# Optimization experiments

Measured on AMD Instinct MI355X. Metric: run time of the kernel, lower is better.

The kernel has to match this reference:

```python
import jax, jax.numpy as jnp
import numpy as np

N = 100000      # nodes
E = 800000      # edges (avg degree 8)
D_IN = 256      # input feature dim
D_H = 256       # hidden dim (hard-coded in module)
D_OUT = 128     # h_feats


def setup_inputs() -> dict:
    key = jax.random.key(0)
    ks = jax.random.split(key, 8)
    feat = jax.random.normal(ks[0], (N, D_IN), jnp.float32)
    src = jax.random.randint(ks[1], (E,), 0, N, dtype=jnp.int32)
    dst = jax.random.randint(ks[2], (E,), 0, N, dtype=jnp.int32)
    def lin(k, din, dout):
        return jax.random.normal(k, (din, dout), jnp.float32) / np.float32(np.sqrt(din))
    return {
        'feat': feat, 'src': src, 'dst': dst,
        'w_self1': lin(ks[3], D_IN, D_H), 'w_neigh1': lin(ks[4], D_IN, D_H),
        'b1': jnp.zeros((D_H,), jnp.float32),
        'w_self2': lin(ks[5], D_H, D_OUT), 'w_neigh2': lin(ks[6], D_H, D_OUT),
        'b2': jnp.zeros((D_OUT,), jnp.float32),
    }


def _sage_mean(h, src, dst, w_self, w_neigh, b):
    # DGL SAGEConv 'mean': rst = h @ W_self + mean_{in-neighbors}(h) @ W_neigh + b
    ones = jnp.ones((src.shape[0],), h.dtype)
    deg = jax.ops.segment_sum(ones, dst, num_segments=N)          # in-degree per node
    msum = jax.ops.segment_sum(h[src], dst, num_segments=N)      # [N, d] gather-scatter
    mean = msum / jnp.maximum(deg, 1.0)[:, None]                  # zero-degree -> 0
    return h @ w_self + mean @ w_neigh + b


def reference(feat, src, dst, w_self1, w_neigh1, b1, w_self2, w_neigh2, b2):
    h = jax.nn.relu(_sage_mean(feat, src, dst, w_self1, w_neigh1, b1))
    h = jax.nn.relu(_sage_mean(h, src, dst, w_self2, w_neigh2, b2))
    # F.normalize(h, dim=1): x / max(||x||_2, eps)
    norm = jnp.linalg.norm(h, axis=1, keepdims=True)
    return h / jnp.maximum(norm, 1e-12)
```

## Files before the change

### kernel.cpp

```cpp
#include <hip/hip_runtime.h>

#define DIN 256
#define DH  256
#define DOUT 128

typedef __attribute__((ext_vector_type(8))) short bf16x8;
typedef __attribute__((ext_vector_type(4))) float f32x4;
typedef __attribute__((ext_vector_type(2))) float f32x2;
typedef __attribute__((ext_vector_type(4))) unsigned short ushort4v;
typedef __attribute__((ext_vector_type(8))) unsigned short ushort8v;
typedef __attribute__((ext_vector_type(4))) unsigned int uint4v;

static __device__ __forceinline__ unsigned short f2bf(float x) {
    unsigned u = __float_as_uint(x);
    u += 0x7fffu + ((u >> 16) & 1u);
    return (unsigned short)(u >> 16);
}
static __device__ __forceinline__ float bf2f(unsigned short h) {
    return __uint_as_float(((unsigned)h) << 16);
}

static __device__ __forceinline__ void gload16(const unsigned short* g, void* l) {
    __builtin_amdgcn_global_load_lds(
        (const __attribute__((address_space(1))) unsigned int*)g,
        (__attribute__((address_space(3))) unsigned int*)l,
        16, 0, 0);
}

__global__ void prep_kernel(const float* __restrict__ feat, unsigned short* __restrict__ featb,
                            unsigned int* __restrict__ feat8, long long nc4,
                            const float* __restrict__ w_self1, const float* __restrict__ w_neigh1,
                            const float* __restrict__ w_self2, const float* __restrict__ w_neigh2,
                            unsigned short* __restrict__ ws1t, unsigned short* __restrict__ wn1t,
                            unsigned short* __restrict__ wcat,
                            const int* __restrict__ dst, int* __restrict__ cnt, int E,
                            int bCvt, int bWt) {
    int b = blockIdx.x;
    if (b < bCvt) {
        long long i = b * 256LL + threadIdx.x;
        if (i >= nc4) return;
        f32x4 v = __builtin_nontemporal_load((const f32x4*)feat + i);
        ushort4v o;
        o[0] = f2bf(v[0]); o[1] = f2bf(v[1]); o[2] = f2bf(v[2]); o[3] = f2bf(v[3]);
        *((ushort4v*)featb + i) = o;
        int u = __builtin_amdgcn_cvt_pk_fp8_f32(v[0], v[1], 0, 0);
        u     = __builtin_amdgcn_cvt_pk_fp8_f32(v[2], v[3], u, 1);
        feat8[i] = (unsigned)u;
    } else if (b < bCvt + bWt) {
        int idx = (b - bCvt) * 256 + threadIdx.x;
        if (idx < 65536) {
            int nn = idx >> 8, k = idx & 255;
            ws1t[idx] = f2bf(w_self1[k * 256 + nn]);
        } else if (idx < 131072) {
            int j = idx - 65536; int nn = j >> 8, k = j & 255;
            wn1t[j] = f2bf(w_neigh1[k * 256 + nn]);
        } else if (idx < 163840) {
            int j = idx - 131072; int nn = j >> 8, k = j & 255;
            wcat[j] = f2bf(w_neigh2[k * 128 + nn]);
        } else if (idx < 196608) {
            int j = idx - 163840; int nn = j >> 8, k = j & 255;
            wcat[32768 + j] = f2bf(w_self2[k * 128 + nn]);
        }
    } else {
        int e = (b - bCvt - bWt) * 256 + threadIdx.x;
        if (e < E) atomicAdd(&cnt[dst[e]], 1);
    }
}

__global__ void block_sums_kernel(const int* __restrict__ cnt, int* __restrict__ partial, int N) {
    __shared__ int sdata[256];
    int t = threadIdx.x;
    int base = blockIdx.x * 1024;
    int s = 0;
#pragma unroll
    for (int j = 0; j < 4; ++j) {
        int i = base + t * 4 + j;
        if (i < N) s += cnt[i];
    }
    sdata[t] = s; __syncthreads();
    for (int o = 128; o; o >>= 1) {
        if (t < o) sdata[t] += sdata[t + o];
        __syncthreads();
    }
    if (t == 0) partial[blockIdx.x] = sdata[0];
}

__global__ void scan_partials_kernel(int* __restrict__ partial, int nb) {
    __shared__ int sdata[256];
    int t = threadIdx.x;
    int v = (t < nb) ? partial[t] : 0;
    sdata[t] = v; __syncthreads();
    for (int o = 1; o < 256; o <<= 1) {
        int y = (t >= o) ? sdata[t - o] : 0;
        __syncthreads();
        sdata[t] += y;
        __syncthreads();
    }
    if (t < nb) partial[t] = sdata[t] - v;
}

__global__ void scan_block_kernel(int* __restrict__ cnt, const int* __restrict__ partial,
                                  int* __restrict__ off, int N, int E) {
    __shared__ int sdata[256];
    int b = blockIdx.x, t = threadIdx.x;
    int base = b * 1024;
    int vals[4]; int local = 0;
#pragma unroll
    for (int j = 0; j < 4; ++j) {
        int i = base + t * 4 + j;
        vals[j] = (i < N) ? cnt[i] : 0;
        local += vals[j];
    }
    sdata[t] = local; __syncthreads();
    for (int o = 1; o < 256; o <<= 1) {
        int y = (t >= o) ? sdata[t - o] : 0;
        __syncthreads();
        sdata[t] += y;
        __syncthreads();
    }
    int run = sdata[t] - local + partial[b];
#pragma unroll
    for (int j = 0; j < 4; ++j) {
        int i = base + t * 4 + j;
        if (i < N) { off[i] = run; cnt[i] = run; }
        run += vals[j];
    }
    if (b == 0 && t == 0) off[N] = E;
}

__global__ void fill_csr_kernel(const int* __restrict__ src, const int* __restrict__ dst,
                                int* __restrict__ cursor, int* __restrict__ csr, int E) {
    int e = blockIdx.x * blockDim.x + threadIdx.x;
    if (e < E) {
        int d = dst[e];
        int p = atomicAdd(&cursor[d], 1);
        csr[p] = src[e];
    }
}

__global__ void gather_mean256_kernel(const unsigned int* __restrict__ feat8, const int* __restrict__ off,
                                      const int* __restrict__ csr, unsigned short* __restrict__ agg, int N) {
    int wid  = (int)((blockIdx.x * (long long)blockDim.x + threadIdx.x) >> 6);
    int lane = threadIdx.x & 63;
    if (wid >= N) return;
    int start = off[wid], end = off[wid + 1];
    const int g   = lane >> 4;
    const int cl  = lane & 15;
    float a[16] = {};
    int e = start;
    for (; e + 7 < end; e += 8) {
        int s0 = csr[e + g], s1 = csr[e + 4 + g];
        uint4v v0 = *(const uint4v*)(feat8 + (long long)s0 * 64 + cl * 4);
        uint4v v1 = *(const uint4v*)(feat8 + (long long)s1 * 64 + cl * 4);
#pragma unroll
        for (int d = 0; d < 4; ++d) {
            f32x2 p0 = __builtin_amdgcn_cvt_pk_f32_fp8((int)v0[d], false);
            f32x2 p1 = __builtin_amdgcn_cvt_pk_f32_fp8((int)v0[d], true);
            f32x2 q0 = __builtin_amdgcn_cvt_pk_f32_fp8((int)v1[d], false);
            f32x2 q1 = __builtin_amdgcn_cvt_pk_f32_fp8((int)v1[d], true);
            a[d * 4 + 0] += p0[0] + q0[0];
            a[d * 4 + 1] += p0[1] + q0[1];
            a[d * 4 + 2] += p1[0] + q1[0];
            a[d * 4 + 3] += p1[1] + q1[1];
        }
    }
    for (; e < end; e += 4) {
        int idx = e + g;
        if (idx < end) {
            int s = csr[idx];
            uint4v v = *(const uint4v*)(feat8 + (long long)s * 64 + cl * 4);
#pragma unroll
            for (int d = 0; d < 4; ++d) {
                f32x2 p0 = __builtin_amdgcn_cvt_pk_f32_fp8((int)v[d], false);
                f32x2 p1 = __builtin_amdgcn_cvt_pk_f32_fp8((int)v[d], true);
                a[d * 4 + 0] += p0[0];
                a[d * 4 + 1] += p0[1];
                a[d * 4 + 2] += p1[0];
                a[d * 4 + 3] += p1[1];
            }
        }
    }
#pragma unroll
    for (int j = 0; j < 16; ++j) {
        a[j] += __shfl_xor(a[j], 16);
        a[j] += __shfl_xor(a[j], 32);
    }
    if (g == 0) {
        float inv = 1.0f / (float)max(end - start, 1);
        ushort8v o0, o1;
#pragma unroll
        for (int j = 0; j < 8; ++j) { o0[j] = f2bf(a[j] * inv); o1[j] = f2bf(a[8 + j] * inv); }
        unsigned short* dstp = agg + (long long)wid * 256 + cl * 16;
        *(ushort8v*)dstp       = o0;
        *(ushort8v*)(dstp + 8) = o1;
    }
}

__global__ __launch_bounds__(512)
void gemm1_kernel(const unsigned short* __restrict__ A,  const unsigned short* __restrict__ WT,
                  const unsigned short* __restrict__ A2, const unsigned short* __restrict__ WT2,
                  const float* __restrict__ bias, unsigned short* __restrict__ C, int M)
{
    const int K = 256;
    __shared__ __align__(16) char lds[2][24576];

    const int tid = threadIdx.x;
    const int wid = tid >> 6, lane = tid & 63;
    const int l15 = lane & 15, lg = lane >> 4;
    const int wr = wid >> 2, wc = wid & 3;
    const int row0 = blockIdx.x * 128;

    long long asrc; int adst;
    {
        int c = tid, r = c >> 2, s = c & 3;
        int kc = s ^ ((r >> 1) & 3);
        asrc = (long long)min(row0 + r, M - 1) * K + kc * 8;
        adst = c * 16;
    }
    long long bsrc[2]; int bdst[2];
#pragma unroll
    for (int i = 0; i < 2; ++i) {
        int c = wid * 128 + i * 64 + lane, r = c >> 2, s = c & 3;
        int kc = s ^ ((r >> 1) & 3);
        bsrc[i] = (long long)r * K + kc * 8;
        bdst[i] = 8192 + c * 16;
    }

    const int slot = (lg ^ ((l15 >> 1) & 3)) * 16;
    int aoff[4], boff[4];
#pragma unroll
    for (int m = 0; m < 4; ++m) aoff[m] = (wr * 64 + m * 16 + l15) * 64 + slot;
#pragma unroll
    for (int n = 0; n < 4; ++n) boff[n] = 8192 + (wc * 64 + n * 16 + l15) * 64 + slot;

    f32x4 acc[4][4] = {};

    auto stage = [&](int buf, int t) {
        const unsigned short* Ap = (t >= 8) ? A2 : A;
        const unsigned short* Wp = (t >= 8) ? WT2 : WT;
        int k0 = (t & 7) * 32;
        gload16(Ap + asrc + k0, &lds[buf][adst]);
        gload16(Wp + bsrc[0] + k0, &lds[buf][bdst[0]]);
        gload16(Wp + bsrc[1] + k0, &lds[buf][bdst[1]]);
    };

    stage(0, 0);
    __syncthreads();

    for (int t = 0; t < 16; ++t) {
        const int cur = t & 1;
        if (t + 1 < 16) stage(cur ^ 1, t + 1);
        const char* L = lds[cur];
        bf16x8 af[4], bfr[4];
#pragma unroll
        for (int m = 0; m < 4; ++m) af[m]  = *(const bf16x8*)(L + aoff[m]);
#pragma unroll
        for (int n = 0; n < 4; ++n) bfr[n] = *(const bf16x8*)(L + boff[n]);
#pragma unroll
        for (int m = 0; m < 4; ++m)
#pragma unroll
            for (int n = 0; n < 4; ++n)
                acc[m][n] = __builtin_amdgcn_mfma_f32_16x16x32_bf16(af[m], bfr[n], acc[m][n], 0, 0, 0);
        __syncthreads();
    }

#pragma unroll
    for (int m = 0; m < 4; ++m) {
#pragma unroll
        for (int rr = 0; rr < 4; ++rr) {
            int grow = row0 + wr * 64 + m * 16 + lg * 4 + rr;
            if (grow >= M) continue;
#pragma unroll
            for (int n = 0; n < 4; ++n) {
                int gcol = wc * 64 + n * 16 + l15;
                float v = fmaxf(acc[m][n][rr] + bias[gcol], 0.f);
                C[(long long)grow * 256 + gcol] = f2bf(v);
            }
        }
    }
}

__global__ __launch_bounds__(512)
void gemm23_kernel(const unsigned short* __restrict__ A, const unsigned short* __restrict__ WT,
                   const float* __restrict__ b2,
                   unsigned short* __restrict__ p2, unsigned short* __restrict__ self2, int M)
{
    const int K = 256;
    __shared__ __align__(16) char lds[2][24576];

    const int tid = threadIdx.x;
    const int wid = tid >> 6, lane = tid & 63;
    const int l15 = lane & 15, lg = lane >> 4;
    const int wr = wid >> 2, wc = wid & 3;
    const int row0 = blockIdx.x * 128;

    long long asrc; int adst;
    {
        int c = tid, r = c >> 2, s = c & 3;
        int kc = s ^ ((r >> 1) & 3);
        asrc = (long long)min(row0 + r, M - 1) * K + kc * 8;
        adst = c * 16;
    }
    long long bsrc[2]; int bdst[2];
#pragma unroll
    for (int i = 0; i < 2; ++i) {
        int c = wid * 128 + i * 64 + lane, r = c >> 2, s = c & 3;
        int kc = s ^ ((r >> 1) & 3);
        bsrc[i] = (long long)r * K + kc * 8;
        bdst[i] = 8192 + c * 16;
    }

    const int slot = (lg ^ ((l15 >> 1) & 3)) * 16;
    int aoff[4], boff[4];
#pragma unroll
    for (int m = 0; m < 4; ++m) aoff[m] = (wr * 64 + m * 16 + l15) * 64 + slot;
#pragma unroll
    for (int n = 0; n < 4; ++n) boff[n] = 8192 + (wc * 64 + n * 16 + l15) * 64 + slot;

    f32x4 acc[4][4] = {};

    auto stage = [&](int buf, int t) {
        int k0 = t * 32;
        gload16(A  + asrc + k0, &lds[buf][adst]);
        gload16(WT + bsrc[0] + k0, &lds[buf][bdst[0]]);
        gload16(WT + bsrc[1] + k0, &lds[buf][bdst[1]]);
    };

    stage(0, 0);
    __syncthreads();

    for (int t = 0; t < 8; ++t) {
        const int cur = t & 1;
        if (t + 1 < 8) stage(cur ^ 1, t + 1);
        const char* L = lds[cur];
        bf16x8 af[4], bfr[4];
#pragma unroll
        for (int m = 0; m < 4; ++m) af[m]  = *(const bf16x8*)(L + aoff[m]);
#pragma unroll
        for (int n = 0; n < 4; ++n) bfr[n] = *(const bf16x8*)(L + boff[n]);
#pragma unroll
        for (int m = 0; m < 4; ++m)
#pragma unroll
            for (int n = 0; n < 4; ++n)
                acc[m][n] = __builtin_amdgcn_mfma_f32_16x16x32_bf16(af[m], bfr[n], acc[m][n], 0, 0, 0);
        __syncthreads();
    }

    if (wc < 2) {
#pragma unroll
        for (int m = 0; m < 4; ++m)
#pragma unroll
            for (int rr = 0; rr < 4; ++rr) {
                int grow = row0 + wr * 64 + m * 16 + lg * 4 + rr;
                if (grow >= M) continue;
#pragma unroll
                for (int n = 0; n < 4; ++n) {
                    int col = wc * 64 + n * 16 + l15;
                    p2[(long long)grow * 128 + col] = f2bf(acc[m][n][rr]);
                }
            }
    } else {
        float bv[4];
#pragma unroll
        for (int n = 0; n < 4; ++n) bv[n] = b2[(wc - 2) * 64 + n * 16 + l15];
#pragma unroll
        for (int m = 0; m < 4; ++m)
#pragma unroll
            for (int rr = 0; rr < 4; ++rr) {
                int grow = row0 + wr * 64 + m * 16 + lg * 4 + rr;
                if (grow >= M) continue;
#pragma unroll
                for (int n = 0; n < 4; ++n) {
                    int col = (wc - 2) * 64 + n * 16 + l15;
                    self2[(long long)grow * 128 + col] = f2bf(acc[m][n][rr] + bv[n]);
                }
            }
    }
}

__global__ void gather_final_kernel(const unsigned short* __restrict__ p2, const int* __restrict__ off,
                                    const int* __restrict__ csr, const unsigned short* __restrict__ self2,
                                    float* __restrict__ out, int N) {
    int wid  = (int)((blockIdx.x * (long long)blockDim.x + threadIdx.x) >> 6);
    int lane = threadIdx.x & 63;
    if (wid >= N) return;
    int start = off[wid], end = off[wid + 1];
    const int g  = lane >> 4;
    const int c8 = (lane & 15) * 8;
    float a[8] = {};
    int e = start;
    for (; e + 7 < end; e += 8) {
        int s0 = csr[e + g], s1 = csr[e + 4 + g];
        ushort8v v0 = *(const ushort8v*)(p2 + (long long)s0 * 128 + c8);
        ushort8v v1 = *(const ushort8v*)(p2 + (long long)s1 * 128 + c8);
#pragma unroll
        for (int j = 0; j < 8; ++j) a[j] += bf2f(v0[j]) + bf2f(v1[j]);
    }
    for (; e < end; e += 4) {
        int idx = e + g;
        if (idx < end) {
            int s = csr[idx];
            ushort8v v = *(const ushort8v*)(p2 + (long long)s * 128 + c8);
#pragma unroll
            for (int j = 0; j < 8; ++j) a[j] += bf2f(v[j]);
        }
    }
#pragma unroll
    for (int j = 0; j < 8; ++j) {
        a[j] += __shfl_xor(a[j], 16);
        a[j] += __shfl_xor(a[j], 32);
    }
    float invd = 1.0f / (float)max(end - start, 1);
    ushort8v sv = *(const ushort8v*)(self2 + (long long)wid * 128 + c8);
    float v[8];
    float ss = 0.f;
#pragma unroll
    for (int j = 0; j < 8; ++j) {
        v[j] = fmaxf(bf2f(sv[j]) + a[j] * invd, 0.f);
        ss += v[j] * v[j];
    }
    ss += __shfl_xor(ss, 1);
    ss += __shfl_xor(ss, 2);
    ss += __shfl_xor(ss, 4);
    ss += __shfl_xor(ss, 8);
    float inv = 1.0f / fmaxf(sqrtf(ss), 1e-12f);
    if (g == 0) {
        f32x4 o0 = { v[0] * inv, v[1] * inv, v[2] * inv, v[3] * inv };
        f32x4 o1 = { v[4] * inv, v[5] * inv, v[6] * inv, v[7] * inv };
        float* dstp = out + (long long)wid * 128 + c8;
        __builtin_nontemporal_store(o0, (f32x4*)dstp);
        __builtin_nontemporal_store(o1, (f32x4*)(dstp + 4));
    }
}

extern "C" void kernel_launch(void* const* d_in, const int* in_sizes, int n_in,
                              void* d_out, int out_size, void* d_ws, size_t ws_size,
                              hipStream_t stream) {
    const float* feat     = (const float*)d_in[0];
    const int*   src      = (const int*)  d_in[1];
    const int*   dst      = (const int*)  d_in[2];
    const float* w_self1  = (const float*)d_in[3];
    const float* w_neigh1 = (const float*)d_in[4];
    const float* b1       = (const float*)d_in[5];
    const float* w_self2  = (const float*)d_in[6];
    const float* w_neigh2 = (const float*)d_in[7];
    const float* b2       = (const float*)d_in[8];
    float* out = (float*)d_out;

    const int N = in_sizes[0] / DIN;
    const int E = in_sizes[1];

    char* ws = (char*)d_ws;
    auto a4k = [](size_t x) { return (x + 4095) & ~(size_t)4095; };
    size_t o = 0;
    int* cnt  = (int*)(ws + o); o += a4k((size_t)N * 4);
    int* off  = (int*)(ws + o); o += a4k((size_t)(N + 1) * 4);
    int* part = (int*)(ws + o); o += a4k(1024);
    int* csr  = (int*)(ws + o); o += a4k((size_t)E * 4);
    unsigned short* ws1t = (unsigned short*)(ws + o); o += a4k((size_t)DIN * DH * 2);
    unsigned short* wn1t = (unsigned short*)(ws + o); o += a4k((size_t)DIN * DH * 2);
    unsigned short* wcat = (unsigned short*)(ws + o); o += a4k((size_t)256 * 256 * 2);
    unsigned int*   feat8 = (unsigned int*)(ws + o); o += a4k((size_t)N * DIN);
    unsigned short* featb = (unsigned short*)(ws + o); o += a4k((size_t)N * DIN * 2);
    unsigned short* aggb  = (unsigned short*)(ws + o); o += a4k((size_t)N * DIN * 2);
    unsigned short* h1b   = (unsigned short*)(ws + o); o += a4k((size_t)N * DH * 2);

    unsigned short* p2b    = featb;
    unsigned short* self2b = aggb;

    const int nblk = (N + 1023) / 1024;

    hipMemsetAsync(cnt, 0, (size_t)N * 4, stream);
    long long nc4 = (long long)N * DIN / 4;
    const int bCvt = (int)((nc4 + 255) / 256);
    const int bWt  = 768;
    const int bCnt = (E + 255) / 256;
    prep_kernel<<<bCvt + bWt + bCnt, 256, 0, stream>>>(
        feat, featb, feat8, nc4, w_self1, w_neigh1, w_self2, w_neigh2,
        ws1t, wn1t, wcat, dst, cnt, E, bCvt, bWt);

    block_sums_kernel<<<nblk, 256, 0, stream>>>(cnt, part, N);
    scan_partials_kernel<<<1, 256, 0, stream>>>(part, nblk);
    scan_block_kernel<<<nblk, 256, 0, stream>>>(cnt, part, off, N, E);
    fill_csr_kernel<<<(E + 255) / 256, 256, 0, stream>>>(src, dst, cnt, csr, E);

    const int mblk = (N + 127) / 128;

    gather_mean256_kernel<<<(N + 3) / 4, 256, 0, stream>>>(feat8, off, csr, aggb, N);
    gemm1_kernel<<<mblk, 512, 0, stream>>>(featb, ws1t, aggb, wn1t, b1, h1b, N);

    gemm23_kernel<<<mblk, 512, 0, stream>>>(h1b, wcat, b2, p2b, self2b, N);
    gather_final_kernel<<<(N + 3) / 4, 256, 0, stream>>>(p2b, off, csr, self2b, out, N);
}
```

Baseline: 287.1 us.

## Merge partial scan into block scan, reorder prep blocks, double per-thread conversion

Removes the single-block scan_partials launch by having every scan_block block redundantly scan the up-to-256 partial sums in shared memory and take its own base. The prep kernel now puts the atomic degree-count blocks first, so the atomics start early, and each conversion thread handles two float4 chunks, which halves the number of conversion blocks. This saves one kernel launch and its serialization at the cost of redundant tiny scans in every block.

```diff
diff --git a/kernel.cpp b/kernel.cpp
--- a/kernel.cpp
+++ b/kernel.cpp
@@ -28,26 +28,19 @@
 }
 
 __global__ void prep_kernel(const float* __restrict__ feat, unsigned short* __restrict__ featb,
-                            unsigned int* __restrict__ feat8, long long nc4,
+                            unsigned int* __restrict__ feat8, long long ncHalf,
                             const float* __restrict__ w_self1, const float* __restrict__ w_neigh1,
                             const float* __restrict__ w_self2, const float* __restrict__ w_neigh2,
                             unsigned short* __restrict__ ws1t, unsigned short* __restrict__ wn1t,
                             unsigned short* __restrict__ wcat,
                             const int* __restrict__ dst, int* __restrict__ cnt, int E,
-                            int bCvt, int bWt) {
+                            int bCnt, int bWt) {
     int b = blockIdx.x;
-    if (b < bCvt) {
-        long long i = b * 256LL + threadIdx.x;
-        if (i >= nc4) return;
-        f32x4 v = __builtin_nontemporal_load((const f32x4*)feat + i);
-        ushort4v o;
-        o[0] = f2bf(v[0]); o[1] = f2bf(v[1]); o[2] = f2bf(v[2]); o[3] = f2bf(v[3]);
-        *((ushort4v*)featb + i) = o;
-        int u = __builtin_amdgcn_cvt_pk_fp8_f32(v[0], v[1], 0, 0);
-        u     = __builtin_amdgcn_cvt_pk_fp8_f32(v[2], v[3], u, 1);
-        feat8[i] = (unsigned)u;
-    } else if (b < bCvt + bWt) {
-        int idx = (b - bCvt) * 256 + threadIdx.x;
+    if (b < bCnt) {
+        int e = b * 256 + threadIdx.x;
+        if (e < E) atomicAdd(&cnt[dst[e]], 1);
+    } else if (b < bCnt + bWt) {
+        int idx = (b - bCnt) * 256 + threadIdx.x;
         if (idx < 65536) {
             int nn = idx >> 8, k = idx & 255;
             ws1t[idx] = f2bf(w_self1[k * 256 + nn]);
@@ -62,8 +55,22 @@
             wcat[32768 + j] = f2bf(w_self2[k * 128 + nn]);
         }
     } else {
-        int e = (b - bCvt - bWt) * 256 + threadIdx.x;
-        if (e < E) atomicAdd(&cnt[dst[e]], 1);
+        long long i = (b - bCnt - bWt) * 256LL + threadIdx.x;
+        if (i >= ncHalf) return;
+        long long i2 = i + ncHalf;
+        f32x4 v0 = __builtin_nontemporal_load((const f32x4*)feat + i);
+        f32x4 v1 = __builtin_nontemporal_load((const f32x4*)feat + i2);
+        ushort4v o0, o1;
+        o0[0] = f2bf(v0[0]); o0[1] = f2bf(v0[1]); o0[2] = f2bf(v0[2]); o0[3] = f2bf(v0[3]);
+        o1[0] = f2bf(v1[0]); o1[1] = f2bf(v1[1]); o1[2] = f2bf(v1[2]); o1[3] = f2bf(v1[3]);
+        *((ushort4v*)featb + i)  = o0;
+        *((ushort4v*)featb + i2) = o1;
+        int u0 = __builtin_amdgcn_cvt_pk_fp8_f32(v0[0], v0[1], 0, 0);
+        u0     = __builtin_amdgcn_cvt_pk_fp8_f32(v0[2], v0[3], u0, 1);
+        int u1 = __builtin_amdgcn_cvt_pk_fp8_f32(v1[0], v1[1], 0, 0);
+        u1     = __builtin_amdgcn_cvt_pk_fp8_f32(v1[2], v1[3], u1, 1);
+        feat8[i]  = (unsigned)u0;
+        feat8[i2] = (unsigned)u1;
     }
 }
 
@@ -85,24 +92,25 @@
     if (t == 0) partial[blockIdx.x] = sdata[0];
 }
 
-__global__ void scan_partials_kernel(int* __restrict__ partial, int nb) {
+__global__ void scan_block_kernel(int* __restrict__ cnt, const int* __restrict__ partial,
+                                  int* __restrict__ off, int N, int E, int nb) {
     __shared__ int sdata[256];
-    int t = threadIdx.x;
-    int v = (t < nb) ? partial[t] : 0;
-    sdata[t] = v; __syncthreads();
+    __shared__ int pbase;
+    int b = blockIdx.x, t = threadIdx.x;
+
+    int pv = (t < nb) ? partial[t] : 0;
+    sdata[t] = pv; __syncthreads();
     for (int o = 1; o < 256; o <<= 1) {
         int y = (t >= o) ? sdata[t - o] : 0;
         __syncthreads();
         sdata[t] += y;
         __syncthreads();
     }
-    if (t < nb) partial[t] = sdata[t] - v;
-}
-
-__global__ void scan_block_kernel(int* __restrict__ cnt, const int* __restrict__ partial,
-                                  int* __restrict__ off, int N, int E) {
-    __shared__ int sdata[256];
-    int b = blockIdx.x, t = threadIdx.x;
+    if (t == 0) pbase = (b == 0) ? 0 : sdata[b - 1];
+    __syncthreads();
+    int base0 = pbase;
+    __syncthreads();
+
     int base = b * 1024;
     int vals[4]; int local = 0;
 #pragma unroll
@@ -118,7 +126,7 @@
         sdata[t] += y;
         __syncthreads();
     }
-    int run = sdata[t] - local + partial[b];
+    int run = sdata[t] - local + base0;
 #pragma unroll
     for (int j = 0; j < 4; ++j) {
         int i = base + t * 4 + j;
@@ -471,17 +479,16 @@
     const int nblk = (N + 1023) / 1024;
 
     hipMemsetAsync(cnt, 0, (size_t)N * 4, stream);
-    long long nc4 = (long long)N * DIN / 4;
-    const int bCvt = (int)((nc4 + 255) / 256);
+    long long ncHalf = (long long)N * DIN / 8;
+    const int bCnt = (E + 255) / 256;
     const int bWt  = 768;
-    const int bCnt = (E + 255) / 256;
-    prep_kernel<<<bCvt + bWt + bCnt, 256, 0, stream>>>(
-        feat, featb, feat8, nc4, w_self1, w_neigh1, w_self2, w_neigh2,
-        ws1t, wn1t, wcat, dst, cnt, E, bCvt, bWt);
+    const int bCvt = (int)((ncHalf + 255) / 256);
+    prep_kernel<<<bCnt + bWt + bCvt, 256, 0, stream>>>(
+        feat, featb, feat8, ncHalf, w_self1, w_neigh1, w_self2, w_neigh2,
+        ws1t, wn1t, wcat, dst, cnt, E, bCnt, bWt);
 
     block_sums_kernel<<<nblk, 256, 0, stream>>>(cnt, part, N);
-    scan_partials_kernel<<<1, 256, 0, stream>>>(part, nblk);
-    scan_block_kernel<<<nblk, 256, 0, stream>>>(cnt, part, off, N, E);
+    scan_block_kernel<<<nblk, 256, 0, stream>>>(cnt, part, off, N, E, nblk);
     fill_csr_kernel<<<(E + 255) / 256, 256, 0, stream>>>(src, dst, cnt, csr, E);
 
     const int mblk = (N + 127) / 128;
```

After: 282.5 us. About the same (-1.6%).
